# Kernel tuning notes

Hardware: AMD Instinct MI355X
Metric: run time of the kernel (lower is better)

## Reference

```python
import jax, jax.numpy as jnp
import numpy as np

HID = 128
CIN = 256


def setup_inputs() -> dict:
    key = jax.random.key(0)
    k1, k2, k3, k4, k5, k6 = jax.random.split(key, 6)
    b, c, h, w = 32, CIN, 32, 32
    left_features = jax.random.normal(k1, (b, c, h, w), dtype=jnp.float32)
    right_features = jax.random.normal(k2, (b, c, h, w), dtype=jnp.float32)
    # 1x1 conv weights (stored as [out_ch, in_ch]) + biases
    Wq = jax.random.normal(k3, (HID, CIN), dtype=jnp.float32) * (1.0 / np.sqrt(CIN))
    bq = jax.random.normal(k4, (HID,), dtype=jnp.float32) * 0.01
    Wk = jax.random.normal(k5, (HID, CIN), dtype=jnp.float32) * (1.0 / np.sqrt(CIN))
    bk = jax.random.normal(k6, (HID,), dtype=jnp.float32) * 0.01
    return {"left_features": left_features, "right_features": right_features,
            "Wq": Wq, "bq": bq, "Wk": Wk, "bk": bk, "vis_CA": 0}


def reference(left_features, right_features, Wq, bq, Wk, bk, vis_CA):
    b, c, h, w = right_features.shape
    # 1x1 convs = per-pixel linear projections
    Q = jnp.einsum('oc,bchw->bohw', Wq, left_features) + bq[None, :, None, None]   # [b,HID,h,w]
    K = jnp.einsum('oc,bchw->bohw', Wk, right_features) + bk[None, :, None, None]  # [b,HID,h,w]
    V = right_features.reshape(b, c, h * w)                                        # [b,c,hw]
    # global cross-attention over all spatial locations
    attn = jnp.einsum('bcij,bckl->bijkl', Q, K).reshape(b, h, w, h * w)            # [b,h,w,hw]
    attn = jax.nn.softmax(attn, axis=3)
    attended = jnp.einsum('bijp,bcp->bcij', attn, V)                               # [b,c,h,w]
    # rearrange([left, attended], 'two b c h w -> b (two c) h w')
    return jnp.concatenate([left_features, attended], axis=1)                      # [b,2c,h,w]
```

## Files before the change

kernel.cpp:

```cpp
#include <hip/hip_runtime.h>
#include <stdint.h>
#include <stddef.h>

#define NPIX  1024
#define DHID  128
#define CIN   256

typedef _Float16 f16;
typedef __attribute__((ext_vector_type(4))) _Float16 f16x4;
typedef __attribute__((ext_vector_type(8))) _Float16 f16x8;
typedef __attribute__((ext_vector_type(4))) float f32x4;
typedef __attribute__((ext_vector_type(16))) float f32x16;

#define MFMA16(a,b,c) __builtin_amdgcn_mfma_f32_16x16x32_f16((a),(b),(c),0,0,0)
#define MFMA32(a,b,c) __builtin_amdgcn_mfma_f32_32x32x16_f16((a),(b),(c),0,0,0)

typedef const __attribute__((address_space(1))) uint32_t GU32;
typedef __attribute__((address_space(3))) uint32_t LU32;

__device__ __forceinline__ void gll16(const void* g, void* l) {
  __builtin_amdgcn_global_load_lds((GU32*)g, (LU32*)l, 16, 0, 0);
}

__global__ void wprep_kernel(const float* __restrict__ Wq, const float* __restrict__ Wk,
                             f16* __restrict__ Whq, f16* __restrict__ Whk) {
  int i = blockIdx.x * 256 + threadIdx.x;
  if (i < DHID * CIN) { Whq[i] = (f16)Wq[i]; Whk[i] = (f16)Wk[i]; }
}

__global__ __launch_bounds__(256) void proj_kernel(
    const float* __restrict__ Xl, const float* __restrict__ Xr,
    const f16* __restrict__ Whq, const f16* __restrict__ Whk,
    const float* __restrict__ bq, const float* __restrict__ bk,
    f16* __restrict__ QT, f16* __restrict__ KT,
    float* __restrict__ out, f16* __restrict__ Vb)
{
  __shared__ f16 sX[32 * 68];
  __shared__ f16 sO[64 * 136];

  const int tid = threadIdx.x;
  const int w = tid >> 6, lane = tid & 63, g = lane >> 4, r16 = lane & 15;
  const int p0 = blockIdx.x * 64, b = blockIdx.y;
  const bool isK = (blockIdx.z != 0);

  const float* X = (isK ? Xr : Xl) + (size_t)b * CIN * NPIX;
  const f16* Wh = isK ? Whk : Whq;
  const float* bias = isK ? bk : bq;
  f16* QKT = (isK ? KT : QT) + (size_t)b * NPIX * DHID;

  f32x4 acc[8];
#pragma unroll
  for (int i = 0; i < 8; ++i)
#pragma unroll
    for (int j = 0; j < 4; ++j) acc[i][j] = 0.f;

  const int scl = tid >> 4;
  const int spl = (tid & 15) * 4;

  for (int c0 = 0; c0 < CIN; c0 += 32) {
    __syncthreads();
#pragma unroll
    for (int i = 0; i < 2; ++i) {
      int cl = scl + 16 * i;
      size_t goff = (size_t)(c0 + cl) * NPIX + p0 + spl;
      f32x4 v = *(const f32x4*)(X + goff);
      if (!isK) *(f32x4*)(out + ((size_t)b * 2 * CIN + c0 + cl) * NPIX + p0 + spl) = v;
      f16x4 hv = {(f16)v.x, (f16)v.y, (f16)v.z, (f16)v.w};
      if (isK) *(f16x4*)(Vb + (size_t)b * CIN * NPIX + goff) = hv;
      *(f16x4*)(&sX[cl * 68 + spl]) = hv;
    }
    __syncthreads();
    f16x8 xb;
#pragma unroll
    for (int j = 0; j < 8; ++j) xb[j] = sX[(8 * g + j) * 68 + 16 * w + r16];
#pragma unroll
    for (int dt = 0; dt < 8; ++dt) {
      f16x8 wa = *(const f16x8*)(Wh + (size_t)(dt * 16 + r16) * CIN + c0 + 8 * g);
      acc[dt] = MFMA16(wa, xb, acc[dt]);
    }
  }

#pragma unroll
  for (int dt = 0; dt < 8; ++dt) {
    f16x4 hv;
#pragma unroll
    for (int r = 0; r < 4; ++r) hv[r] = (f16)(acc[dt][r] + bias[dt * 16 + 4 * g + r]);
    *(f16x4*)(&sO[(16 * w + r16) * 136 + dt * 16 + 4 * g]) = hv;
  }
  __syncthreads();
  const int pr = tid >> 2, dseg = (tid & 3) * 32;
#pragma unroll
  for (int i = 0; i < 4; ++i) {
    f16x8 row = *(const f16x8*)(&sO[pr * 136 + dseg + 8 * i]);
    *(f16x8*)(QKT + (size_t)(p0 + pr) * DHID + dseg + 8 * i) = row;
  }
}

__global__ __launch_bounds__(256) void attn_kernel(
    const f16* __restrict__ QT, const f16* __restrict__ KT,
    const f16* __restrict__ Vb, float* __restrict__ out)
{
  __shared__ f16 sK[2][64 * 128];
  __shared__ f16 sP[4][32 * 64];

  const int tid = threadIdx.x;
  const int w = tid >> 6, lane = tid & 63;
  const int h = lane >> 5, l31 = lane & 31;
  const int b = blockIdx.x & 31, qt = blockIdx.x >> 5;
  const int q0 = qt * 128 + w * 32;

  const f16* QTb = QT + ((size_t)b * NPIX + q0 + l31) * DHID;
  const f16* KTb = KT + (size_t)b * NPIX * DHID;
  const f16* vBb = Vb + (size_t)b * CIN * NPIX;

  f16x8 qf[8];
#pragma unroll
  for (int kt = 0; kt < 8; ++kt) qf[kt] = *(const f16x8*)(QTb + 16 * kt + 8 * h);

  f32x16 oacc[8];
#pragma unroll
  for (int i = 0; i < 8; ++i)
#pragma unroll
    for (int j = 0; j < 16; ++j) oacc[i][j] = 0.f;

  float mrun = -3.0e38f, lrun = 0.f;
  const int swz = (l31 & 7) << 4;

#define STAGE(kvt, buf)                                                        \
  {                                                                            \
    _Pragma("unroll")                                                          \
    for (int i = 0; i < 4; ++i) {                                              \
      int chunk = tid + 256 * i;                                               \
      int row = chunk >> 4, cc = chunk & 15;                                   \
      gll16(KTb + (size_t)((kvt) + row) * DHID + ((cc ^ (row & 7)) * 8),       \
            &sK[buf][chunk * 8]);                                              \
    }                                                                          \
  }

  STAGE(0, 0);
  __syncthreads();

  for (int t = 0; t < 16; ++t) {
    const int cur = t & 1;
    if (t < 15) STAGE((t + 1) * 64, cur ^ 1);

    f32x16 s0, s1;
#pragma unroll
    for (int j = 0; j < 16; ++j) { s0[j] = 0.f; s1[j] = 0.f; }
    const char* sKc = (const char*)&sK[cur][0];
#pragma unroll
    for (int kt = 0; kt < 8; ++kt) {
      int cb = 32 * kt + 16 * h;
      f16x8 k0 = *(const f16x8*)(sKc + l31 * 256 + (cb ^ swz));
      f16x8 k1 = *(const f16x8*)(sKc + (32 + l31) * 256 + (cb ^ swz));
      s0 = MFMA32(k0, qf[kt], s0);
      s1 = MFMA32(k1, qf[kt], s1);
    }

    float pmax = -3.4e38f;
#pragma unroll
    for (int j = 0; j < 16; ++j) { pmax = fmaxf(pmax, s0[j]); pmax = fmaxf(pmax, s1[j]); }
    pmax = fmaxf(pmax, __shfl_xor(pmax, 32));
    if (__any(pmax > mrun + 8.f)) {
      float mnew = fmaxf(mrun, pmax);
      float sc = __expf(mrun - mnew);
      lrun *= sc; mrun = mnew;
#pragma unroll
      for (int i = 0; i < 8; ++i)
#pragma unroll
        for (int j = 0; j < 16; ++j) oacc[i][j] *= sc;
    }
    float psum = 0.f;
    char* sPw = (char*)&sP[w][0];
#pragma unroll
    for (int pt = 0; pt < 2; ++pt) {
#pragma unroll
      for (int rq = 0; rq < 4; ++rq) {
        const f32x16& s = pt ? s1 : s0;
        float e0 = __expf(s[4 * rq + 0] - mrun), e1 = __expf(s[4 * rq + 1] - mrun);
        float e2 = __expf(s[4 * rq + 2] - mrun), e3 = __expf(s[4 * rq + 3] - mrun);
        psum += e0 + e1 + e2 + e3;
        f16x4 p4 = {(f16)e0, (f16)e1, (f16)e2, (f16)e3};
        int p = 32 * pt + 8 * rq + 4 * h;
        *(f16x4*)(sPw + l31 * 128 + ((p * 2) ^ swz)) = p4;
      }
    }
    psum += __shfl_xor(psum, 32);
    lrun += psum;

    f16x8 pf[4];
#pragma unroll
    for (int pk = 0; pk < 4; ++pk)
      pf[pk] = *(const f16x8*)(sPw + l31 * 128 + (((16 * pk + 8 * h) * 2) ^ swz));
#pragma unroll
    for (int ct = 0; ct < 8; ++ct) {
      const f16* vrow = vBb + (size_t)(32 * ct + l31) * NPIX + t * 64 + 8 * h;
#pragma unroll
      for (int pk = 0; pk < 4; ++pk) {
        f16x8 vf = *(const f16x8*)(vrow + 16 * pk);
        oacc[ct] = MFMA32(vf, pf[pk], oacc[ct]);
      }
    }
    __syncthreads();
  }

  float inv = 1.f / lrun;
  float* ob = out + ((size_t)b * 2 * CIN + CIN) * NPIX + q0 + l31;
#pragma unroll
  for (int ct = 0; ct < 8; ++ct)
#pragma unroll
    for (int r = 0; r < 16; ++r) {
      int c = 32 * ct + (r & 3) + 8 * (r >> 2) + 4 * h;
      ob[(size_t)c * NPIX] = oacc[ct][r] * inv;
    }
}

extern "C" void kernel_launch(void* const* d_in, const int* in_sizes, int n_in,
                              void* d_out, int out_size, void* d_ws, size_t ws_size,
                              hipStream_t stream) {
  const float* left  = (const float*)d_in[0];
  const float* right = (const float*)d_in[1];
  const float* Wq    = (const float*)d_in[2];
  const float* bq    = (const float*)d_in[3];
  const float* Wk    = (const float*)d_in[4];
  const float* bk    = (const float*)d_in[5];
  float* out = (float*)d_out;
  char* ws = (char*)d_ws;

  f16* Whq = (f16*)(ws);
  f16* Whk = (f16*)(ws + 65536);
  size_t off = 131072;
  const size_t QSZ = (size_t)32 * NPIX * DHID * sizeof(f16);
  f16* QT = (f16*)(ws + off); off += QSZ;
  f16* KT = (f16*)(ws + off); off += QSZ;
  f16* Vb = (f16*)(ws + off); off += (size_t)32 * CIN * NPIX * sizeof(f16);
  (void)ws_size; (void)in_sizes; (void)n_in; (void)out_size;

  wprep_kernel<<<128, 256, 0, stream>>>(Wq, Wk, Whq, Whk);

  dim3 pgrid(16, 32, 2);
  proj_kernel<<<pgrid, 256, 0, stream>>>(left, right, Whq, Whk, bq, bk,
                                         QT, KT, out, Vb);

  attn_kernel<<<256, 256, 0, stream>>>(QT, KT, Vb, out);
}
```

Measured before the change: 235.4 us.

## Split attention blocks across channel dimension and restage projection input once

The attention kernel now gives each block 32 queries, with the four waves splitting the 256 output channels instead of each wave owning separate queries. That raises the grid from 256 to 1024 blocks, cuts the per-wave output accumulators from eight tiles to two, and maps blocks to batches so neighbours share K/V in cache. Each wave now computes a quarter of the 128-key score tile, so the softmax max and sum go through shared memory with extra block barriers per tile. The K staging is no longer double-buffered, and the projection kernel loads all 256 input channels into a transposed, swizzled shared tile once instead of looping over channel chunks with repeated barriers.

```diff
diff --git a/kernel.cpp b/kernel.cpp
--- a/kernel.cpp
+++ b/kernel.cpp
@@ -35,8 +35,9 @@
     f16* __restrict__ QT, f16* __restrict__ KT,
     float* __restrict__ out, f16* __restrict__ Vb)
 {
-  __shared__ f16 sX[32 * 68];
-  __shared__ f16 sO[64 * 136];
+  __shared__ char smem[64 * 264 * 2];
+  f16* sXT = (f16*)smem;
+  f16* sO  = (f16*)smem;
 
   const int tid = threadIdx.x;
   const int w = tid >> 6, lane = tid & 63, g = lane >> 4, r16 = lane & 15;
@@ -48,37 +49,44 @@
   const float* bias = isK ? bk : bq;
   f16* QKT = (isK ? KT : QT) + (size_t)b * NPIX * DHID;
 
+  const int cl = tid >> 4;
+  const int p4 = (tid & 15) * 4;
+  const int csw = (tid & 3) << 3;
+#pragma unroll
+  for (int i = 0; i < 16; ++i) {
+    int c = cl + 16 * i;
+    f32x4 v = *(const f32x4*)(X + (size_t)c * NPIX + p0 + p4);
+    if (!isK) *(f32x4*)(out + ((size_t)b * 2 * CIN + c) * NPIX + p0 + p4) = v;
+    f16x4 hv = {(f16)v.x, (f16)v.y, (f16)v.z, (f16)v.w};
+    if (isK) *(f16x4*)(Vb + ((size_t)b * CIN + c) * NPIX + p0 + p4) = hv;
+    int cs = c ^ csw;
+#pragma unroll
+    for (int j = 0; j < 4; ++j) sXT[(p4 + j) * 264 + cs] = hv[j];
+  }
+  __syncthreads();
+
+  const int prow = 16 * w + r16;
+  const int swzp = ((r16 >> 2) & 3) << 3;
+  f16x8 xb[8];
+#pragma unroll
+  for (int kc = 0; kc < 8; ++kc)
+    xb[kc] = *(const f16x8*)(sXT + prow * 264 + ((kc * 32 + 8 * g) ^ swzp));
+
   f32x4 acc[8];
 #pragma unroll
   for (int i = 0; i < 8; ++i)
 #pragma unroll
     for (int j = 0; j < 4; ++j) acc[i][j] = 0.f;
 
-  const int scl = tid >> 4;
-  const int spl = (tid & 15) * 4;
-
-  for (int c0 = 0; c0 < CIN; c0 += 32) {
-    __syncthreads();
-#pragma unroll
-    for (int i = 0; i < 2; ++i) {
-      int cl = scl + 16 * i;
-      size_t goff = (size_t)(c0 + cl) * NPIX + p0 + spl;
-      f32x4 v = *(const f32x4*)(X + goff);
-      if (!isK) *(f32x4*)(out + ((size_t)b * 2 * CIN + c0 + cl) * NPIX + p0 + spl) = v;
-      f16x4 hv = {(f16)v.x, (f16)v.y, (f16)v.z, (f16)v.w};
-      if (isK) *(f16x4*)(Vb + (size_t)b * CIN * NPIX + goff) = hv;
-      *(f16x4*)(&sX[cl * 68 + spl]) = hv;
-    }
-    __syncthreads();
-    f16x8 xb;
-#pragma unroll
-    for (int j = 0; j < 8; ++j) xb[j] = sX[(8 * g + j) * 68 + 16 * w + r16];
+#pragma unroll
+  for (int kc = 0; kc < 8; ++kc)
 #pragma unroll
     for (int dt = 0; dt < 8; ++dt) {
-      f16x8 wa = *(const f16x8*)(Wh + (size_t)(dt * 16 + r16) * CIN + c0 + 8 * g);
-      acc[dt] = MFMA16(wa, xb, acc[dt]);
-    }
-  }
+      f16x8 wa = *(const f16x8*)(Wh + (size_t)(dt * 16 + r16) * CIN + kc * 32 + 8 * g);
+      acc[dt] = MFMA16(wa, xb[kc], acc[dt]);
+    }
+
+  __syncthreads();
 
 #pragma unroll
   for (int dt = 0; dt < 8; ++dt) {
@@ -100,14 +108,16 @@
     const f16* __restrict__ QT, const f16* __restrict__ KT,
     const f16* __restrict__ Vb, float* __restrict__ out)
 {
-  __shared__ f16 sK[2][64 * 128];
-  __shared__ f16 sP[4][32 * 64];
+  __shared__ f16 sK[128 * 128];
+  __shared__ f16 sP[32 * 128];
+  __shared__ float sM[4][32], sL[4][32];
 
   const int tid = threadIdx.x;
   const int w = tid >> 6, lane = tid & 63;
   const int h = lane >> 5, l31 = lane & 31;
-  const int b = blockIdx.x & 31, qt = blockIdx.x >> 5;
-  const int q0 = qt * 128 + w * 32;
+  const int x = blockIdx.x;
+  const int b = (x & 7) * 4 + ((x >> 3) & 3);
+  const int q0 = (x >> 5) * 32;
 
   const f16* QTb = QT + ((size_t)b * NPIX + q0 + l31) * DHID;
   const f16* KTb = KT + (size_t)b * NPIX * DHID;
@@ -117,88 +127,91 @@
 #pragma unroll
   for (int kt = 0; kt < 8; ++kt) qf[kt] = *(const f16x8*)(QTb + 16 * kt + 8 * h);
 
-  f32x16 oacc[8];
-#pragma unroll
-  for (int i = 0; i < 8; ++i)
-#pragma unroll
-    for (int j = 0; j < 16; ++j) oacc[i][j] = 0.f;
-
-  float mrun = -3.0e38f, lrun = 0.f;
-  const int swz = (l31 & 7) << 4;
-
-#define STAGE(kvt, buf)                                                        \
+#define STAGE(tt)                                                              \
   {                                                                            \
     _Pragma("unroll")                                                          \
-    for (int i = 0; i < 4; ++i) {                                              \
+    for (int i = 0; i < 8; ++i) {                                              \
       int chunk = tid + 256 * i;                                               \
       int row = chunk >> 4, cc = chunk & 15;                                   \
-      gll16(KTb + (size_t)((kvt) + row) * DHID + ((cc ^ (row & 7)) * 8),       \
-            &sK[buf][chunk * 8]);                                              \
+      gll16(KTb + (size_t)((tt) * 128 + row) * DHID + ((cc ^ (row & 7)) * 8),  \
+            &sK[chunk * 8]);                                                   \
     }                                                                          \
   }
 
-  STAGE(0, 0);
-  __syncthreads();
-
-  for (int t = 0; t < 16; ++t) {
-    const int cur = t & 1;
-    if (t < 15) STAGE((t + 1) * 64, cur ^ 1);
-
-    f32x16 s0, s1;
-#pragma unroll
-    for (int j = 0; j < 16; ++j) { s0[j] = 0.f; s1[j] = 0.f; }
-    const char* sKc = (const char*)&sK[cur][0];
+  f32x16 oacc[2];
+#pragma unroll
+  for (int i = 0; i < 2; ++i)
+#pragma unroll
+    for (int j = 0; j < 16; ++j) oacc[i][j] = 0.f;
+  float mrun = -3.0e38f, lrun = 0.f;
+
+  const int swzq = (l31 & 7) << 4;
+  char* sPq = (char*)sP + l31 * 256;
+
+  STAGE(0);
+  __syncthreads();
+
+  for (int t = 0; t < 8; ++t) {
+    const int r = 32 * w + l31;
+    const int swzr = (l31 & 7) << 4;
+    const char* sKc = (const char*)sK;
+    f32x16 s;
+#pragma unroll
+    for (int j = 0; j < 16; ++j) s[j] = 0.f;
 #pragma unroll
     for (int kt = 0; kt < 8; ++kt) {
-      int cb = 32 * kt + 16 * h;
-      f16x8 k0 = *(const f16x8*)(sKc + l31 * 256 + (cb ^ swz));
-      f16x8 k1 = *(const f16x8*)(sKc + (32 + l31) * 256 + (cb ^ swz));
-      s0 = MFMA32(k0, qf[kt], s0);
-      s1 = MFMA32(k1, qf[kt], s1);
-    }
-
-    float pmax = -3.4e38f;
-#pragma unroll
-    for (int j = 0; j < 16; ++j) { pmax = fmaxf(pmax, s0[j]); pmax = fmaxf(pmax, s1[j]); }
-    pmax = fmaxf(pmax, __shfl_xor(pmax, 32));
-    if (__any(pmax > mrun + 8.f)) {
-      float mnew = fmaxf(mrun, pmax);
+      f16x8 kf = *(const f16x8*)(sKc + r * 256 + ((32 * kt + 16 * h) ^ swzr));
+      s = MFMA32(kf, qf[kt], s);
+    }
+
+    float m_w = s[0];
+#pragma unroll
+    for (int j = 1; j < 16; ++j) m_w = fmaxf(m_w, s[j]);
+    m_w = fmaxf(m_w, __shfl_xor(m_w, 32));
+    if (lane < 32) sM[w][lane] = m_w;
+    __syncthreads();
+
+    if (t < 7) STAGE(t + 1);
+
+    float m_tile = fmaxf(fmaxf(sM[0][l31], sM[1][l31]),
+                         fmaxf(sM[2][l31], sM[3][l31]));
+    if (__any(m_tile > mrun + 8.f)) {
+      float mnew = fmaxf(mrun, m_tile);
       float sc = __expf(mrun - mnew);
       lrun *= sc; mrun = mnew;
 #pragma unroll
-      for (int i = 0; i < 8; ++i)
+      for (int i = 0; i < 2; ++i)
 #pragma unroll
         for (int j = 0; j < 16; ++j) oacc[i][j] *= sc;
     }
+
     float psum = 0.f;
-    char* sPw = (char*)&sP[w][0];
-#pragma unroll
-    for (int pt = 0; pt < 2; ++pt) {
-#pragma unroll
-      for (int rq = 0; rq < 4; ++rq) {
-        const f32x16& s = pt ? s1 : s0;
-        float e0 = __expf(s[4 * rq + 0] - mrun), e1 = __expf(s[4 * rq + 1] - mrun);
-        float e2 = __expf(s[4 * rq + 2] - mrun), e3 = __expf(s[4 * rq + 3] - mrun);
-        psum += e0 + e1 + e2 + e3;
-        f16x4 p4 = {(f16)e0, (f16)e1, (f16)e2, (f16)e3};
-        int p = 32 * pt + 8 * rq + 4 * h;
-        *(f16x4*)(sPw + l31 * 128 + ((p * 2) ^ swz)) = p4;
+#pragma unroll
+    for (int r4 = 0; r4 < 4; ++r4) {
+      f16x4 p4v;
+#pragma unroll
+      for (int j = 0; j < 4; ++j) {
+        float pe = __expf(s[4 * r4 + j] - mrun);
+        psum += pe; p4v[j] = (f16)pe;
       }
+      *(f16x4*)(sPq + (((64 * w + 16 * r4 + 8 * h)) ^ swzq)) = p4v;
     }
     psum += __shfl_xor(psum, 32);
-    lrun += psum;
-
-    f16x8 pf[4];
-#pragma unroll
-    for (int pk = 0; pk < 4; ++pk)
-      pf[pk] = *(const f16x8*)(sPw + l31 * 128 + (((16 * pk + 8 * h) * 2) ^ swz));
-#pragma unroll
-    for (int ct = 0; ct < 8; ++ct) {
-      const f16* vrow = vBb + (size_t)(32 * ct + l31) * NPIX + t * 64 + 8 * h;
-#pragma unroll
-      for (int pk = 0; pk < 4; ++pk) {
-        f16x8 vf = *(const f16x8*)(vrow + 16 * pk);
-        oacc[ct] = MFMA32(vf, pf[pk], oacc[ct]);
+    if (lane < 32) sL[w][lane] = psum;
+    __syncthreads();
+    lrun += sL[0][l31] + sL[1][l31] + sL[2][l31] + sL[3][l31];
+
+    f16x8 pf[8];
+#pragma unroll
+    for (int km = 0; km < 8; ++km)
+      pf[km] = *(const f16x8*)(sPq + ((32 * km + 16 * h) ^ swzq));
+#pragma unroll
+    for (int ct = 0; ct < 2; ++ct) {
+      const f16* vrow = vBb + (size_t)(64 * w + 32 * ct + l31) * NPIX + 128 * t + 8 * h;
+#pragma unroll
+      for (int km = 0; km < 8; ++km) {
+        f16x8 vf = *(const f16x8*)(vrow + 16 * km);
+        oacc[ct] = MFMA32(vf, pf[km], oacc[ct]);
       }
     }
     __syncthreads();
@@ -207,11 +220,11 @@
   float inv = 1.f / lrun;
   float* ob = out + ((size_t)b * 2 * CIN + CIN) * NPIX + q0 + l31;
 #pragma unroll
-  for (int ct = 0; ct < 8; ++ct)
-#pragma unroll
-    for (int r = 0; r < 16; ++r) {
-      int c = 32 * ct + (r & 3) + 8 * (r >> 2) + 4 * h;
-      ob[(size_t)c * NPIX] = oacc[ct][r] * inv;
+  for (int ct = 0; ct < 2; ++ct)
+#pragma unroll
+    for (int rg = 0; rg < 16; ++rg) {
+      int c = 64 * w + 32 * ct + (rg & 3) + 8 * (rg >> 2) + 4 * h;
+      ob[(size_t)c * NPIX] = oacc[ct][rg] * inv;
     }
 }
 
@@ -242,5 +255,5 @@
   proj_kernel<<<pgrid, 256, 0, stream>>>(left, right, Whq, Whk, bq, bk,
                                          QT, KT, out, Vb);
 
-  attn_kernel<<<256, 256, 0, stream>>>(QT, KT, Vb, out);
-}
+  attn_kernel<<<1024, 256, 0, stream>>>(QT, KT, Vb, out);
+}
```

Result: no change. 236.6 us (+0.5%).
